# Optimization experiments

Measured on AMD Instinct MI355X. Metric: run time of the kernel, lower is better.

## Reference

```python
import jax, jax.numpy as jnp
import numpy as np

HEADS = 12
HEAD_DIM = 64
WINDOW = 65  # must be odd
EMBED = 768
B, L = 1, 2048


def setup_inputs() -> dict:
    key = jax.random.key(0)
    k1, k2, k3 = jax.random.split(key, 3)
    x = jax.random.normal(k1, (B, L, EMBED), dtype=jnp.float32)
    w_qkv = jax.random.normal(k2, (EMBED, 3 * HEADS * HEAD_DIM), dtype=jnp.float32) * 0.02
    w_out = jax.random.normal(k3, (HEADS * HEAD_DIM, EMBED), dtype=jnp.float32) * 0.02
    b_out = jnp.zeros((EMBED,), dtype=jnp.float32)
    return {"x": x, "w_qkv": w_qkv, "w_out": w_out, "b_out": b_out}


def reference(x, w_qkv, w_out, b_out):
    b, l, _ = x.shape
    pad = WINDOW // 2
    # qkv projection (no bias), reshape to [B, L, H, 3*Dh], split as in TF code
    qkv = jnp.einsum('ble,ef->blf', x, w_qkv).reshape(b, l, HEADS, 3 * HEAD_DIM)
    q = qkv[..., :HEAD_DIM]                      # [B, L, H, Dh]
    k = qkv[..., HEAD_DIM:2 * HEAD_DIM]
    v = qkv[..., 2 * HEAD_DIM:]
    # zero-pad along sequence (matches tf.pad; padded positions participate in softmax)
    k_pad = jnp.pad(k, ((0, 0), (pad, pad), (0, 0), (0, 0)))  # [B, L+2p, H, Dh]
    v_pad = jnp.pad(v, ((0, 0), (pad, pad), (0, 0), (0, 0)))
    # sliding windows via a single gather: [B, L, W, H, Dh]
    idx = jnp.arange(l)[:, None] + jnp.arange(WINDOW)[None, :]
    k_win = k_pad[:, idx]
    v_win = v_pad[:, idx]
    score = jnp.einsum('blhd,blwhd->blhw', q, k_win) / jnp.sqrt(
        jnp.asarray(HEAD_DIM, dtype=x.dtype))
    weights = jax.nn.softmax(score, axis=-1)      # [B, L, H, W]
    out = jnp.einsum('blhw,blwhd->blhd', weights, v_win)
    out = out.reshape(b, l, HEADS * HEAD_DIM)
    return jnp.einsum('blf,fe->ble', out, w_out) + b_out
```

## Files before the change

### kernel.cpp

```cpp
#include <hip/hip_runtime.h>
#include <hip/hip_bf16.h>

#define HEADS 12
#define HD 64
#define PADW 32
#define EMBED 768
#define LSEQ 2048
#define QKV_N (3 * HEADS * HD)
#define LPAD (LSEQ + 64)

typedef short short8 __attribute__((ext_vector_type(8)));
typedef short short4v __attribute__((ext_vector_type(4)));
typedef float f32x4 __attribute__((ext_vector_type(4)));

__device__ short g_xb[LSEQ * EMBED];
__device__ short g_wqkvT[QKV_N * EMBED];
__device__ short g_woutT[EMBED * EMBED];
__device__ short g_qkvb[LSEQ * QKV_N];
__device__ short g_vT[HEADS * HD * LPAD];
__device__ short g_attnb[LSEQ * EMBED];

__device__ __forceinline__ short f2bf(float f) {
  unsigned x = __builtin_bit_cast(unsigned, f);
  x += 0x7fffu + ((x >> 16) & 1u);
  return (short)(x >> 16);
}

#define GLB(p) ((const __attribute__((address_space(1))) void*)(p))
#define LDS(p) ((__attribute__((address_space(3))) void*)(p))

#define PREP_A 1536
#define PREP_B 1728
#define PREP_C 576
#define PREP_D 24
#define PREP_TOT (PREP_A + PREP_B + PREP_C + PREP_D)

__global__ __launch_bounds__(256) void prep(
    const float* __restrict__ x, const float* __restrict__ w_qkv,
    const float* __restrict__ w_out, short* __restrict__ xb,
    short* __restrict__ wqkvT, short* __restrict__ woutT,
    short* __restrict__ vT) {
  __shared__ float T[32][33];
  const int b = blockIdx.x, tid = threadIdx.x;
  if (b < PREP_A) {
    int i = b * 256 + tid;
    float4 v = ((const float4*)x)[i];
    short4v o;
    o[0] = f2bf(v.x); o[1] = f2bf(v.y); o[2] = f2bf(v.z); o[3] = f2bf(v.w);
    ((short4v*)xb)[i] = o;
  } else if (b < PREP_A + PREP_B + PREP_C) {
    const float* W; short* WT; int N, bx, by;
    if (b < PREP_A + PREP_B) {
      int t = b - PREP_A; W = w_qkv; WT = wqkvT; N = QKV_N; bx = t % 72; by = t / 72;
    } else {
      int t = b - PREP_A - PREP_B; W = w_out; WT = woutT; N = EMBED; bx = t % 24; by = t / 24;
    }
    const int K = EMBED;
    int tx = tid & 31, ty = tid >> 5;
    int n0 = bx * 32, k0 = by * 32;
#pragma unroll
    for (int p = 0; p < 4; ++p)
      T[ty + p * 8][tx] = W[(size_t)(k0 + ty + p * 8) * N + n0 + tx];
    __syncthreads();
#pragma unroll
    for (int p = 0; p < 4; ++p)
      WT[(size_t)(n0 + ty + p * 8) * K + k0 + tx] = f2bf(T[tx][ty + p * 8]);
  } else {
    int j = (b - PREP_A - PREP_B - PREP_C) * 256 + tid;
    int hd = j >> 3, side = (j >> 2) & 1, off = (j & 3) * 8;
    short8 z = {};
    *(short8*)&vT[(size_t)hd * LPAD + side * 2080 + off] = z;
  }
}

template <bool OUT_BF16, bool FUSE_VT>
__global__ __launch_bounds__(256) void gemm_pipe64(
    const short* __restrict__ A, const short* __restrict__ Bt,
    const float* __restrict__ bias, void* __restrict__ Cv,
    short* __restrict__ vT, int M, int N, int K) {
  constexpr int BUF = 2 * 64 * 64;
  constexpr int EPI = OUT_BF16 ? 64 * 80 : 64 * 72 * 2;
  constexpr int LDSZ = (3 * BUF > EPI) ? 3 * BUF : EPI;
  __shared__ __align__(16) short lds_s[LDSZ];

  const int tid = threadIdx.x;
  const int wv = tid >> 6, lane = tid & 63;
  const int wm = wv >> 1, wn = wv & 1;
  const int lanelo = lane & 15, quad = lane >> 4;
  const int m0 = blockIdx.y * 64, n0 = blockIdx.x * 64;
  const int srow8 = lane >> 3, schk = lane & 7;
  const int sgc = schk ^ srow8;
  const int xk = lanelo & 7;

  f32x4 acc[2][2] = {};

  auto stage = [&](int j, int buf) {
    short* Ab = lds_s + buf * BUF;
    short* Bb = Ab + 64 * 64;
    const int k0 = j * 64;
#pragma unroll
    for (int c = 0; c < 2; ++c) {
      int row = wv * 16 + c * 8 + srow8;
      const short* ga = A + (size_t)(m0 + row) * K + k0 + sgc * 8;
      __builtin_amdgcn_global_load_lds(GLB(ga), LDS(&Ab[(wv * 16 + c * 8) * 64]), 16, 0, 0);
    }
#pragma unroll
    for (int c = 0; c < 2; ++c) {
      int row = wv * 16 + c * 8 + srow8;
      const short* gb = Bt + (size_t)(n0 + row) * K + k0 + sgc * 8;
      __builtin_amdgcn_global_load_lds(GLB(gb), LDS(&Bb[(wv * 16 + c * 8) * 64]), 16, 0, 0);
    }
  };

  auto compute = [&](int buf) {
    short* Ab = lds_s + buf * BUF;
    short* Bb = Ab + 64 * 64;
    short8 af[2][2], bfr[2][2];
#pragma unroll
    for (int ks = 0; ks < 2; ++ks) {
#pragma unroll
      for (int mt = 0; mt < 2; ++mt) {
        int row = wm * 32 + mt * 16 + lanelo;
        int p = (ks * 4 + quad) ^ xk;
        af[ks][mt] = *(const short8*)&Ab[row * 64 + p * 8];
      }
#pragma unroll
      for (int nt = 0; nt < 2; ++nt) {
        int row = wn * 32 + nt * 16 + lanelo;
        int p = (ks * 4 + quad) ^ xk;
        bfr[ks][nt] = *(const short8*)&Bb[row * 64 + p * 8];
      }
    }
    asm volatile("s_waitcnt lgkmcnt(0)" ::: "memory");
#pragma unroll
    for (int ks = 0; ks < 2; ++ks)
#pragma unroll
      for (int mt = 0; mt < 2; ++mt)
#pragma unroll
        for (int nt = 0; nt < 2; ++nt)
          acc[mt][nt] = __builtin_amdgcn_mfma_f32_16x16x32_bf16(
              af[ks][mt], bfr[ks][nt], acc[mt][nt], 0, 0, 0);
  };

  const int steps = K / 64;
  stage(0, 0);
  stage(1, 1);
  int cur = 0;
  for (int j = 0; j < steps - 1; ++j) {
    asm volatile("s_waitcnt vmcnt(4)" ::: "memory");
    asm volatile("s_barrier" ::: "memory");
    if (j + 2 < steps) {
      int b2 = cur + 2; if (b2 >= 3) b2 -= 3;
      stage(j + 2, b2);
    }
    compute(cur);
    ++cur; if (cur == 3) cur = 0;
  }
  asm volatile("s_waitcnt vmcnt(0)" ::: "memory");
  asm volatile("s_barrier" ::: "memory");
  compute(cur);

  if (FUSE_VT) {
#pragma unroll
    for (int nt = 0; nt < 2; ++nt) {
      int c0 = n0 + wn * 32 + nt * 16;
      if ((c0 % 192) >= 128) {
        int h = c0 / 192, d0 = (c0 % 192) - 128;
#pragma unroll
        for (int mt = 0; mt < 2; ++mt) {
          int d = d0 + lanelo;
          int row0 = m0 + wm * 32 + mt * 16 + quad * 4;
          short4v o;
#pragma unroll
          for (int r = 0; r < 4; ++r) o[r] = f2bf(acc[mt][nt][r]);
          *(short4v*)&vT[(size_t)(h * 64 + d) * LPAD + PADW + row0] = o;
        }
      }
    }
  }

  __syncthreads();
  if (OUT_BF16) {
    constexpr int ST = 80;
#pragma unroll
    for (int mt = 0; mt < 2; ++mt)
#pragma unroll
      for (int nt = 0; nt < 2; ++nt) {
        int rloc = wm * 32 + mt * 16 + quad * 4;
        int cloc = wn * 32 + nt * 16 + lanelo;
#pragma unroll
        for (int r = 0; r < 4; ++r)
          lds_s[(rloc + r) * ST + cloc] = f2bf(acc[mt][nt][r]);
      }
    __syncthreads();
    short* Cc = (short*)Cv;
#pragma unroll
    for (int rp = 0; rp < 64; rp += 32) {
      int row = rp + tid / 8, seg = tid % 8;
      short8 vv = *(const short8*)&lds_s[row * ST + seg * 8];
      *(short8*)&Cc[(size_t)(m0 + row) * N + n0 + seg * 8] = vv;
    }
  } else {
    constexpr int ST = 72;
    float* fl = (float*)lds_s;
#pragma unroll
    for (int mt = 0; mt < 2; ++mt)
#pragma unroll
      for (int nt = 0; nt < 2; ++nt) {
        int rloc = wm * 32 + mt * 16 + quad * 4;
        int cloc = wn * 32 + nt * 16 + lanelo;
#pragma unroll
        for (int r = 0; r < 4; ++r)
          fl[(rloc + r) * ST + cloc] = acc[mt][nt][r];
      }
    __syncthreads();
    float* Cc = (float*)Cv;
#pragma unroll
    for (int rp = 0; rp < 64; rp += 16) {
      int row = rp + tid / 16, seg = tid % 16;
      float4 vv = *(const float4*)&fl[row * ST + seg * 4];
      float4 bb = *(const float4*)&bias[n0 + seg * 4];
      vv.x += bb.x; vv.y += bb.y; vv.z += bb.z; vv.w += bb.w;
      *(float4*)&Cc[(size_t)(m0 + row) * N + n0 + seg * 4] = vv;
    }
  }
}

__global__ __launch_bounds__(256) void attn_mfma(
    const short* __restrict__ qkvb, const short* __restrict__ vT,
    short* __restrict__ attnb) {
  const int blk = blockIdx.x;
  const int h = blk % HEADS;
  const int l0 = (blk / HEADS) * 64;
  const int sb = l0 - PADW;

  const int tid = threadIdx.x;
  const int wv = tid >> 6, lane = tid & 63;
  const int lanelo = lane & 15, quad = lane >> 4;
  const int qoff = h * 192, koff = h * 192 + 64;

  __shared__ __align__(16) short P_lds[64 * 136];

  const short* qp = qkvb + (size_t)(l0 + wv * 16 + lanelo) * QKV_N + qoff;
  short8 aq0 = *(const short8*)(qp + quad * 8);
  short8 aq1 = *(const short8*)(qp + 32 + quad * 8);

  f32x4 sacc[8] = {};
#pragma unroll
  for (int nt = 0; nt < 8; ++nt) {
    int gl = sb + nt * 16 + lanelo;
    short8 bk0 = {}, bk1 = {};
    if ((unsigned)gl < (unsigned)LSEQ) {
      const short* kp = qkvb + (size_t)gl * QKV_N + koff;
      bk0 = *(const short8*)(kp + quad * 8);
      bk1 = *(const short8*)(kp + 32 + quad * 8);
    }
    sacc[nt] = __builtin_amdgcn_mfma_f32_16x16x32_bf16(aq0, bk0, sacc[nt], 0, 0, 0);
    sacc[nt] = __builtin_amdgcn_mfma_f32_16x16x32_bf16(aq1, bk1, sacc[nt], 0, 0, 0);
  }

  short8 bv[4][4];
#pragma unroll
  for (int ks = 0; ks < 4; ++ks) {
    int lp = l0 + ks * 32 + quad * 8;
#pragma unroll
    for (int nt = 0; nt < 4; ++nt) {
      int d = nt * 16 + lanelo;
      bv[ks][nt] = *(const short8*)&vT[((size_t)h * 64 + d) * LPAD + lp];
    }
  }

  float rsum[4] = {0.f, 0.f, 0.f, 0.f};
#pragma unroll
  for (int nt = 0; nt < 8; ++nt)
#pragma unroll
    for (int r = 0; r < 4; ++r) {
      int li = wv * 16 + quad * 4 + r;
      int widx = nt * 16 + lanelo - li;
      float s = (widx >= 0 && widx <= 64) ? sacc[nt][r] * 0.125f : -1e30f;
      float p = __expf(s);
      sacc[nt][r] = p;
      rsum[r] += p;
    }
#pragma unroll
  for (int r = 0; r < 4; ++r) {
#pragma unroll
    for (int off = 1; off < 16; off <<= 1)
      rsum[r] += __shfl_xor(rsum[r], off);
    rsum[r] = 1.f / rsum[r];
  }
#pragma unroll
  for (int nt = 0; nt < 8; ++nt)
#pragma unroll
    for (int r = 0; r < 4; ++r) {
      int row = wv * 16 + quad * 4 + r;
      P_lds[row * 136 + nt * 16 + lanelo] = f2bf(sacc[nt][r] * rsum[r]);
    }
  __syncthreads();

  f32x4 oacc[4] = {};
#pragma unroll
  for (int ks = 0; ks < 4; ++ks) {
    short8 ap = *(const short8*)&P_lds[(wv * 16 + lanelo) * 136 + ks * 32 + quad * 8];
#pragma unroll
    for (int nt = 0; nt < 4; ++nt)
      oacc[nt] = __builtin_amdgcn_mfma_f32_16x16x32_bf16(ap, bv[ks][nt], oacc[nt], 0, 0, 0);
  }

  __syncthreads();
#pragma unroll
  for (int nt = 0; nt < 4; ++nt)
#pragma unroll
    for (int r = 0; r < 4; ++r) {
      int row = wv * 16 + quad * 4 + r;
      P_lds[row * 80 + nt * 16 + lanelo] = f2bf(oacc[nt][r]);
    }
  __syncthreads();
#pragma unroll
  for (int rp = 0; rp < 64; rp += 32) {
    int row = rp + tid / 8, seg = tid % 8;
    short8 vv = *(const short8*)&P_lds[row * 80 + seg * 8];
    *(short8*)&attnb[(size_t)(l0 + row) * EMBED + h * 64 + seg * 8] = vv;
  }
}

extern "C" void kernel_launch(void* const* d_in, const int* in_sizes, int n_in,
                              void* d_out, int out_size, void* d_ws, size_t ws_size,
                              hipStream_t stream) {
  const float* x     = (const float*)d_in[0];
  const float* w_qkv = (const float*)d_in[1];
  const float* w_out = (const float*)d_in[2];
  const float* b_out = (const float*)d_in[3];
  float* out = (float*)d_out;

  short *xb, *wqkvT, *woutT, *qkvb, *vT, *attnb;
  (void)hipGetSymbolAddress((void**)&xb,    HIP_SYMBOL(g_xb));
  (void)hipGetSymbolAddress((void**)&wqkvT, HIP_SYMBOL(g_wqkvT));
  (void)hipGetSymbolAddress((void**)&woutT, HIP_SYMBOL(g_woutT));
  (void)hipGetSymbolAddress((void**)&qkvb,  HIP_SYMBOL(g_qkvb));
  (void)hipGetSymbolAddress((void**)&vT,    HIP_SYMBOL(g_vT));
  (void)hipGetSymbolAddress((void**)&attnb, HIP_SYMBOL(g_attnb));

  prep<<<PREP_TOT, 256, 0, stream>>>(x, w_qkv, w_out, xb, wqkvT, woutT, vT);

  gemm_pipe64<true, true><<<dim3(QKV_N / 64, LSEQ / 64), 256, 0, stream>>>(
      xb, wqkvT, nullptr, qkvb, vT, LSEQ, QKV_N, EMBED);

  attn_mfma<<<(LSEQ / 64) * HEADS, 256, 0, stream>>>(qkvb, vT, attnb);

  gemm_pipe64<false, false><<<dim3(EMBED / 64, LSEQ / 64), 256, 0, stream>>>(
      attnb, woutT, b_out, out, nullptr, LSEQ, EMBED, EMBED);
}
```

Baseline: 112.8 us.

## Make GEMM warps load private tiles and drop block barriers

```diff
diff --git a/kernel.cpp b/kernel.cpp
--- a/kernel.cpp
+++ b/kernel.cpp
@@ -74,64 +74,65 @@
 }
 
 template <bool OUT_BF16, bool FUSE_VT>
-__global__ __launch_bounds__(256) void gemm_pipe64(
+__global__ __launch_bounds__(256) void gemm_wp64(
     const short* __restrict__ A, const short* __restrict__ Bt,
     const float* __restrict__ bias, void* __restrict__ Cv,
     short* __restrict__ vT, int M, int N, int K) {
-  constexpr int BUF = 2 * 64 * 64;
-  constexpr int EPI = OUT_BF16 ? 64 * 80 : 64 * 72 * 2;
-  constexpr int LDSZ = (3 * BUF > EPI) ? 3 * BUF : EPI;
-  __shared__ __align__(16) short lds_s[LDSZ];
+  __shared__ __align__(16) short lds_s[4 * 2 * 4096];
 
   const int tid = threadIdx.x;
   const int wv = tid >> 6, lane = tid & 63;
   const int wm = wv >> 1, wn = wv & 1;
   const int lanelo = lane & 15, quad = lane >> 4;
-  const int m0 = blockIdx.y * 64, n0 = blockIdx.x * 64;
+  const int m0 = blockIdx.y * 64 + wm * 32;
+  const int n0 = blockIdx.x * 64 + wn * 32;
   const int srow8 = lane >> 3, schk = lane & 7;
   const int sgc = schk ^ srow8;
   const int xk = lanelo & 7;
+  short* wlds = lds_s + wv * 2 * 4096;
 
   f32x4 acc[2][2] = {};
 
   auto stage = [&](int j, int buf) {
-    short* Ab = lds_s + buf * BUF;
-    short* Bb = Ab + 64 * 64;
+    short* Ab = wlds + buf * 4096;
+    short* Bb = Ab + 2048;
     const int k0 = j * 64;
 #pragma unroll
-    for (int c = 0; c < 2; ++c) {
-      int row = wv * 16 + c * 8 + srow8;
+    for (int c = 0; c < 4; ++c) {
+      int row = c * 8 + srow8;
       const short* ga = A + (size_t)(m0 + row) * K + k0 + sgc * 8;
-      __builtin_amdgcn_global_load_lds(GLB(ga), LDS(&Ab[(wv * 16 + c * 8) * 64]), 16, 0, 0);
-    }
-#pragma unroll
-    for (int c = 0; c < 2; ++c) {
-      int row = wv * 16 + c * 8 + srow8;
+      __builtin_amdgcn_global_load_lds(GLB(ga), LDS(&Ab[c * 8 * 64]), 16, 0, 0);
+    }
+#pragma unroll
+    for (int c = 0; c < 4; ++c) {
+      int row = c * 8 + srow8;
       const short* gb = Bt + (size_t)(n0 + row) * K + k0 + sgc * 8;
-      __builtin_amdgcn_global_load_lds(GLB(gb), LDS(&Bb[(wv * 16 + c * 8) * 64]), 16, 0, 0);
+      __builtin_amdgcn_global_load_lds(GLB(gb), LDS(&Bb[c * 8 * 64]), 16, 0, 0);
     }
   };
 
-  auto compute = [&](int buf) {
-    short* Ab = lds_s + buf * BUF;
-    short* Bb = Ab + 64 * 64;
+  const int steps = K / 64;
+  stage(0, 0);
+  stage(1, 1);
+  for (int j = 0; j < steps; ++j) {
+    const int buf = j & 1;
+    if (j < steps - 1) asm volatile("s_waitcnt vmcnt(8)" ::: "memory");
+    else               asm volatile("s_waitcnt vmcnt(0)" ::: "memory");
+    short* Ab = wlds + buf * 4096;
+    short* Bb = Ab + 2048;
     short8 af[2][2], bfr[2][2];
 #pragma unroll
     for (int ks = 0; ks < 2; ++ks) {
-#pragma unroll
-      for (int mt = 0; mt < 2; ++mt) {
-        int row = wm * 32 + mt * 16 + lanelo;
-        int p = (ks * 4 + quad) ^ xk;
-        af[ks][mt] = *(const short8*)&Ab[row * 64 + p * 8];
-      }
-#pragma unroll
-      for (int nt = 0; nt < 2; ++nt) {
-        int row = wn * 32 + nt * 16 + lanelo;
-        int p = (ks * 4 + quad) ^ xk;
-        bfr[ks][nt] = *(const short8*)&Bb[row * 64 + p * 8];
-      }
+      int p = (ks * 4 + quad) ^ xk;
+#pragma unroll
+      for (int mt = 0; mt < 2; ++mt)
+        af[ks][mt] = *(const short8*)&Ab[(mt * 16 + lanelo) * 64 + p * 8];
+#pragma unroll
+      for (int nt = 0; nt < 2; ++nt)
+        bfr[ks][nt] = *(const short8*)&Bb[(nt * 16 + lanelo) * 64 + p * 8];
     }
     asm volatile("s_waitcnt lgkmcnt(0)" ::: "memory");
+    if (j + 2 < steps) stage(j + 2, buf);
 #pragma unroll
     for (int ks = 0; ks < 2; ++ks)
 #pragma unroll
@@ -140,36 +141,18 @@
         for (int nt = 0; nt < 2; ++nt)
           acc[mt][nt] = __builtin_amdgcn_mfma_f32_16x16x32_bf16(
               af[ks][mt], bfr[ks][nt], acc[mt][nt], 0, 0, 0);
-  };
-
-  const int steps = K / 64;
-  stage(0, 0);
-  stage(1, 1);
-  int cur = 0;
-  for (int j = 0; j < steps - 1; ++j) {
-    asm volatile("s_waitcnt vmcnt(4)" ::: "memory");
-    asm volatile("s_barrier" ::: "memory");
-    if (j + 2 < steps) {
-      int b2 = cur + 2; if (b2 >= 3) b2 -= 3;
-      stage(j + 2, b2);
-    }
-    compute(cur);
-    ++cur; if (cur == 3) cur = 0;
-  }
-  asm volatile("s_waitcnt vmcnt(0)" ::: "memory");
-  asm volatile("s_barrier" ::: "memory");
-  compute(cur);
+  }
 
   if (FUSE_VT) {
 #pragma unroll
     for (int nt = 0; nt < 2; ++nt) {
-      int c0 = n0 + wn * 32 + nt * 16;
+      int c0 = n0 + nt * 16;
       if ((c0 % 192) >= 128) {
         int h = c0 / 192, d0 = (c0 % 192) - 128;
 #pragma unroll
         for (int mt = 0; mt < 2; ++mt) {
           int d = d0 + lanelo;
-          int row0 = m0 + wm * 32 + mt * 16 + quad * 4;
+          int row0 = m0 + mt * 16 + quad * 4;
           short4v o;
 #pragma unroll
           for (int r = 0; r < 4; ++r) o[r] = f2bf(acc[mt][nt][r]);
@@ -179,45 +162,47 @@
     }
   }
 
-  __syncthreads();
   if (OUT_BF16) {
-    constexpr int ST = 80;
+    constexpr int ST = 40;
+    short* eb = wlds;
 #pragma unroll
     for (int mt = 0; mt < 2; ++mt)
 #pragma unroll
       for (int nt = 0; nt < 2; ++nt) {
-        int rloc = wm * 32 + mt * 16 + quad * 4;
-        int cloc = wn * 32 + nt * 16 + lanelo;
+        int rloc = mt * 16 + quad * 4;
+        int cloc = nt * 16 + lanelo;
 #pragma unroll
         for (int r = 0; r < 4; ++r)
-          lds_s[(rloc + r) * ST + cloc] = f2bf(acc[mt][nt][r]);
+          eb[(rloc + r) * ST + cloc] = f2bf(acc[mt][nt][r]);
       }
-    __syncthreads();
+    asm volatile("s_waitcnt lgkmcnt(0)" ::: "memory");
     short* Cc = (short*)Cv;
 #pragma unroll
-    for (int rp = 0; rp < 64; rp += 32) {
-      int row = rp + tid / 8, seg = tid % 8;
-      short8 vv = *(const short8*)&lds_s[row * ST + seg * 8];
+    for (int pass = 0; pass < 2; ++pass) {
+      int u = pass * 64 + lane;
+      int row = u >> 2, seg = u & 3;
+      short8 vv = *(const short8*)&eb[row * ST + seg * 8];
       *(short8*)&Cc[(size_t)(m0 + row) * N + n0 + seg * 8] = vv;
     }
   } else {
-    constexpr int ST = 72;
-    float* fl = (float*)lds_s;
+    constexpr int ST = 36;
+    float* fl = (float*)wlds;
 #pragma unroll
     for (int mt = 0; mt < 2; ++mt)
 #pragma unroll
       for (int nt = 0; nt < 2; ++nt) {
-        int rloc = wm * 32 + mt * 16 + quad * 4;
-        int cloc = wn * 32 + nt * 16 + lanelo;
+        int rloc = mt * 16 + quad * 4;
+        int cloc = nt * 16 + lanelo;
 #pragma unroll
         for (int r = 0; r < 4; ++r)
           fl[(rloc + r) * ST + cloc] = acc[mt][nt][r];
       }
-    __syncthreads();
+    asm volatile("s_waitcnt lgkmcnt(0)" ::: "memory");
     float* Cc = (float*)Cv;
 #pragma unroll
-    for (int rp = 0; rp < 64; rp += 16) {
-      int row = rp + tid / 16, seg = tid % 16;
+    for (int pass = 0; pass < 4; ++pass) {
+      int u = pass * 64 + lane;
+      int row = u >> 3, seg = u & 7;
       float4 vv = *(const float4*)&fl[row * ST + seg * 4];
       float4 bb = *(const float4*)&bias[n0 + seg * 4];
       vv.x += bb.x; vv.y += bb.y; vv.z += bb.z; vv.w += bb.w;
@@ -343,11 +328,11 @@
 
   prep<<<PREP_TOT, 256, 0, stream>>>(x, w_qkv, w_out, xb, wqkvT, woutT, vT);
 
-  gemm_pipe64<true, true><<<dim3(QKV_N / 64, LSEQ / 64), 256, 0, stream>>>(
+  gemm_wp64<true, true><<<dim3(QKV_N / 64, LSEQ / 64), 256, 0, stream>>>(
       xb, wqkvT, nullptr, qkvb, vT, LSEQ, QKV_N, EMBED);
 
   attn_mfma<<<(LSEQ / 64) * HEADS, 256, 0, stream>>>(qkvb, vT, attnb);
 
-  gemm_pipe64<false, false><<<dim3(EMBED / 64, LSEQ / 64), 256, 0, stream>>>(
+  gemm_wp64<false, false><<<dim3(EMBED / 64, LSEQ / 64), 256, 0, stream>>>(
       attnb, woutT, b_out, out, nullptr, LSEQ, EMBED, EMBED);
 }
```

Measured after the change: 110.7 us, median of 2. No clear change (-1.8%).
